# Kernel optimization log

Measured on AMD Instinct MI355X. Metric: run time of the kernel, lower is better.

The kernel has to match this reference:

```python
import jax, jax.numpy as jnp
import numpy as np
import math

B, T, C = 1, 4096, 2048
N_HEAD, N_KV = 16, 4
HD = C // N_HEAD            # 128
QPK = N_HEAD // N_KV        # 4
WINDOW = 1024
QKV_OUT = (N_HEAD + 2 * N_KV) * HD  # 3072


def setup_inputs() -> dict:
    key = jax.random.key(0)
    k1, k2, k3 = jax.random.split(key, 3)
    x = jax.random.normal(k1, (B, T, C), dtype=jnp.float32)
    W_attn = jax.random.normal(k2, (C, QKV_OUT), dtype=jnp.float32) * 0.02
    W_proj = jax.random.normal(k3, (C, C), dtype=jnp.float32) * 0.02
    # RoPE table: (T, HD//2, 2) = (cos, sin)
    inv_freq = 1.0 / (10000.0 ** (np.arange(0, HD, 2, dtype=np.float32) / HD))
    t = np.arange(T, dtype=np.float32)
    ang = np.outer(t, inv_freq)  # (T, HD//2)
    freqs_cis = jnp.asarray(np.stack([np.cos(ang), np.sin(ang)], axis=-1))
    return {"x": x, "freqs_cis": freqs_cis, "W_attn": W_attn, "W_proj": W_proj}


def apply_rope(xh, freqs_cis):
    # xh: (B, T, H, D); freqs_cis: (T, D//2, 2)
    b, t, h, d = xh.shape
    xs = xh.astype(jnp.float32).reshape(b, t, h, d // 2, 2)
    fc = freqs_cis.reshape(1, t, 1, d // 2, 2)
    re = xs[..., 0] * fc[..., 0] - xs[..., 1] * fc[..., 1]
    im = xs[..., 1] * fc[..., 0] + xs[..., 0] * fc[..., 1]
    return jnp.stack([re, im], axis=-1).reshape(b, t, h, d).astype(xh.dtype)


def reference(x, freqs_cis, W_attn, W_proj):
    qkv = x @ W_attn                                    # (B, T, 3072)
    tot = QPK + 2
    qkv = qkv.reshape(B, T, N_KV, tot, HD)
    qkv = jnp.transpose(qkv, (0, 2, 3, 1, 4))           # (B, n_kv, tot, T, hd)
    q = qkv[:, :, :QPK]                                 # (B, n_kv, qpk, T, hd)
    k = qkv[:, :, QPK:QPK + 1]
    v = qkv[:, :, QPK + 1:]
    # Faithful to torch: raw contiguous reshape (scrambles head/time layout)
    q = q.reshape(B, -1, N_HEAD, HD)                    # (B, T, n_head, hd)
    k = k.reshape(B, -1, N_KV, HD)
    v = v.reshape(B, -1, N_KV, HD)
    q = apply_rope(q, freqs_cis)
    k = apply_rope(k, freqs_cis)
    # GQA: physical repeat_interleave of K/V heads
    k = jnp.repeat(k, QPK, axis=2)                      # (B, T, n_head, hd)
    v = jnp.repeat(v, QPK, axis=2)
    q = jnp.transpose(q, (0, 2, 1, 3))                  # (B, n_head, T, hd)
    k = jnp.transpose(k, (0, 2, 1, 3))
    v = jnp.transpose(v, (0, 2, 1, 3))
    scores = jnp.einsum("bhqd,bhkd->bhqk", q, k) / math.sqrt(HD)
    # Symmetric band mask (triu(-w+1) * tril(w-1)): |i-j| <= w-1. NOT causal.
    i = jnp.arange(T)[:, None]
    j = jnp.arange(T)[None, :]
    band = jnp.abs(i - j) <= (WINDOW - 1)               # (T, T) bool
    scores = jnp.where(band[None, None], scores, -jnp.inf)
    probs = jax.nn.softmax(scores.astype(jnp.float32), axis=-1).astype(q.dtype)
    y = jnp.einsum("bhqk,bhkd->bhqd", probs, v)         # (B, n_head, T, hd)
    y = jnp.transpose(y, (0, 2, 1, 3)).reshape(B, T, C)
    return y @ W_proj
```

## Files before the change

kernel.cpp:

```cpp
#include <hip/hip_runtime.h>
#include <hip/hip_bf16.h>

typedef __attribute__((ext_vector_type(8))) short short8;
typedef __attribute__((ext_vector_type(4))) float f32x4;

static constexpr int Tt   = 4096;
static constexpr int Cc   = 2048;
static constexpr int NH   = 16;
static constexpr int HD   = 128;
static constexpr int QKVO = 3072;
static constexpr int W1   = 1023;

#define GLDS16(gp, lp)                                                        \
  __builtin_amdgcn_global_load_lds(                                           \
      (const __attribute__((address_space(1))) unsigned int*)(gp),            \
      (__attribute__((address_space(3))) unsigned int*)(lp), 16, 0, 0)

__global__ void cvt4(const float* __restrict__ in,
                     __hip_bfloat16* __restrict__ out, int n) {
  int i = (blockIdx.x * blockDim.x + threadIdx.x) * 4;
  if (i >= n) return;
  float4 v = *(const float4*)&in[i];
  union { ushort4 u; __hip_bfloat16 b[4]; } o;
  o.b[0] = __float2bfloat16(v.x);
  o.b[1] = __float2bfloat16(v.y);
  o.b[2] = __float2bfloat16(v.z);
  o.b[3] = __float2bfloat16(v.w);
  *(ushort4*)&out[i] = o.u;
}

__global__ void tconv(const float* __restrict__ W,
                      __hip_bfloat16* __restrict__ Wt, int K, int N) {
  __shared__ float tile[32][33];
  const int k0 = blockIdx.x * 32, n0 = blockIdx.y * 32;
  const int tx = threadIdx.x, ty = threadIdx.y;
#pragma unroll
  for (int r = 0; r < 4; ++r)
    tile[ty * 4 + r][tx] = W[(size_t)(k0 + ty * 4 + r) * N + n0 + tx];
  __syncthreads();
#pragma unroll
  for (int r = 0; r < 4; ++r)
    Wt[(size_t)(n0 + ty * 4 + r) * K + k0 + tx] =
        __float2bfloat16(tile[tx][ty * 4 + r]);
}

template <bool OUT_BF16>
__global__ __launch_bounds__(256) void gemm_bt(
    const __hip_bfloat16* __restrict__ A, const __hip_bfloat16* __restrict__ Bt,
    void* __restrict__ Cout, int M, int N, int K) {
  __shared__ __hip_bfloat16 As[128 * 32];
  __shared__ __hip_bfloat16 Bs[128 * 32];
  const int tid = threadIdx.x;
  const int lane = tid & 63, wid = tid >> 6;
  const int l15 = lane & 15, lhi = lane >> 4;
  const int m0 = blockIdx.y * 128, n0 = blockIdx.x * 128;
  const int wm = wid >> 1, wn = wid & 1;
  f32x4 acc[4][4] = {};
  for (int k0 = 0; k0 < K; k0 += 32) {
#pragma unroll
    for (int cc = 0; cc < 2; ++cc) {
      const int ebase = cc * 2048 + wid * 512;
      const int el = ebase + lane * 8;
      const int row = el >> 5, col = el & 31;
      GLDS16(A + (size_t)(m0 + row) * K + k0 + col, As + ebase);
      GLDS16(Bt + (size_t)(n0 + row) * K + k0 + col, Bs + ebase);
    }
    __syncthreads();
    short8 af[4], bfr[4];
#pragma unroll
    for (int i = 0; i < 4; ++i)
      af[i] = *(const short8*)&As[(wm * 64 + i * 16 + l15) * 32 + lhi * 8];
#pragma unroll
    for (int j = 0; j < 4; ++j)
      bfr[j] = *(const short8*)&Bs[(wn * 64 + j * 16 + l15) * 32 + lhi * 8];
#pragma unroll
    for (int i = 0; i < 4; ++i)
#pragma unroll
      for (int j = 0; j < 4; ++j)
        acc[i][j] = __builtin_amdgcn_mfma_f32_16x16x32_bf16(af[i], bfr[j],
                                                            acc[i][j], 0, 0, 0);
    __syncthreads();
  }
#pragma unroll
  for (int i = 0; i < 4; ++i)
#pragma unroll
    for (int r = 0; r < 4; ++r) {
      const int row = m0 + wm * 64 + i * 16 + lhi * 4 + r;
#pragma unroll
      for (int j = 0; j < 4; ++j) {
        const int col = n0 + wn * 64 + j * 16 + l15;
        if (OUT_BF16)
          ((__hip_bfloat16*)Cout)[(size_t)row * N + col] =
              __float2bfloat16(acc[i][j][r]);
        else
          ((float*)Cout)[(size_t)row * N + col] = acc[i][j][r];
      }
    }
}

__global__ void rope_scatter(const __hip_bfloat16* __restrict__ qkv,
                             const float* __restrict__ fc,
                             __hip_bfloat16* __restrict__ qb,
                             __hip_bfloat16* __restrict__ kb,
                             __hip_bfloat16* __restrict__ vb) {
  const int p = blockIdx.x * blockDim.x + threadIdx.x;
  const int t = blockIdx.y;
  const int c = p * 2;
  const int kv = c / 768;
  const int rem = c - kv * 768;
  const int slot = rem >> 7;
  const int d = rem & 127;
  const ushort2 xy = *(const ushort2*)&qkv[(size_t)t * QKVO + c];
  const float x0 = __bfloat162float(*(const __hip_bfloat16*)&xy.x);
  const float x1 = __bfloat162float(*(const __hip_bfloat16*)&xy.y);
  union { ushort2 uu; __hip_bfloat16 b[2]; } o;
  if (slot < 4) {
    const unsigned u = ((unsigned)kv << 14) | ((unsigned)slot << 12) | (unsigned)t;
    const int tp = u >> 4, h = u & 15;
    const float2 cs = *(const float2*)&fc[(size_t)tp * 128 + (d >> 1) * 2];
    o.b[0] = __float2bfloat16(x0 * cs.x - x1 * cs.y);
    o.b[1] = __float2bfloat16(x1 * cs.x + x0 * cs.y);
    *(ushort2*)&qb[(size_t)tp * Cc + h * HD + d] = o.uu;
  } else {
    const unsigned u2 = ((unsigned)kv << 12) | (unsigned)t;
    const int tp = u2 >> 2, hk = u2 & 3;
    if (slot == 4) {
      const float2 cs = *(const float2*)&fc[(size_t)tp * 128 + (d >> 1) * 2];
      o.b[0] = __float2bfloat16(x0 * cs.x - x1 * cs.y);
      o.b[1] = __float2bfloat16(x1 * cs.x + x0 * cs.y);
      *(ushort2*)&kb[(size_t)tp * 512 + hk * HD + d] = o.uu;
    } else {
      o.uu = xy;
      *(ushort2*)&vb[(size_t)tp * 512 + hk * HD + d] = o.uu;
    }
  }
}

__global__ __launch_bounds__(512) void attn_band(
    const __hip_bfloat16* __restrict__ qb, const __hip_bfloat16* __restrict__ kb,
    const __hip_bfloat16* __restrict__ vb, __hip_bfloat16* __restrict__ yb) {
  __shared__ __hip_bfloat16 kt[64 * 128];
  __shared__ __hip_bfloat16 vt[128 * 64];
  __shared__ __hip_bfloat16 pl[8][16 * 64];
  const int tid = threadIdx.x, lane = tid & 63, wid = tid >> 6;
  const int l15 = lane & 15, lhi = lane >> 4;
  const int q0 = blockIdx.x * 128, h = blockIdx.y;
  const int kvh = h >> 2;
  const int qrow = q0 + wid * 16 + l15;
  short8 aq[4];
#pragma unroll
  for (int kc = 0; kc < 4; ++kc)
    aq[kc] = *(const short8*)&qb[(size_t)qrow * Cc + h * HD + kc * 32 + lhi * 8];
  f32x4 o[8] = {};
  float mrow[4] = {-1e30f, -1e30f, -1e30f, -1e30f};
  float lrow[4] = {0.f, 0.f, 0.f, 0.f};
  const int js = (q0 - W1 > 0 ? q0 - W1 : 0) & ~63;
  const int jeu = q0 + 128 + W1;
  const int je = jeu < Tt ? jeu : Tt;
  const float scale = 0.08838834764831845f;
  char* ktc = (char*)kt;
  char* vtc = (char*)vt;
  char* plc = (char*)&pl[wid][0];
  for (int j0 = js; j0 < je; j0 += 64) {
    __syncthreads();
#pragma unroll
    for (int cc = 0; cc < 2; ++cc) {
      const int sb = (cc * 8 + wid) << 10;
      const int S = sb + lane * 16;
      const int row = S >> 8;
      const int colb = (S & 255) ^ ((row & 7) << 4);
      int jc = j0 + row;
      jc = jc < Tt - 1 ? jc : Tt - 1;
      GLDS16(kb + (size_t)jc * 512 + kvh * HD + (colb >> 1), ktc + sb);
    }
#pragma unroll
    for (int it = 0; it < 2; ++it) {
      const int d = tid & 127;
      const int jg = (tid >> 7) + it * 4;
      union { short8 v8; unsigned short u[8]; } pk;
#pragma unroll
      for (int q = 0; q < 8; ++q) {
        int jc = j0 + jg * 8 + q;
        jc = jc < Tt - 1 ? jc : Tt - 1;
        pk.u[q] = *(const unsigned short*)&vb[(size_t)jc * 512 + kvh * HD + d];
      }
      const int vbyt = (d * 128 + jg * 16) ^ ((d & 7) << 4);
      *(short8*)(vtc + vbyt) = pk.v8;
    }
    __syncthreads();
    f32x4 s[4] = {};
#pragma unroll
    for (int jt = 0; jt < 4; ++jt) {
      const int row = jt * 16 + l15;
      const int sw = (row & 7) << 4;
#pragma unroll
      for (int kc = 0; kc < 4; ++kc) {
        const short8 bk =
            *(const short8*)(ktc + row * 256 + ((kc * 64 + lhi * 16) ^ sw));
        s[jt] = __builtin_amdgcn_mfma_f32_16x16x32_bf16(aq[kc], bk, s[jt], 0, 0, 0);
      }
    }
    float val[4][4], pm[4];
#pragma unroll
    for (int jt = 0; jt < 4; ++jt)
#pragma unroll
      for (int r = 0; r < 4; ++r) {
        const int j = j0 + jt * 16 + l15;
        const int i = q0 + wid * 16 + lhi * 4 + r;
        const int diff = i > j ? i - j : j - i;
        const bool ok = (j < Tt) && (diff <= W1);
        val[jt][r] = ok ? s[jt][r] * scale : -1e30f;
      }
#pragma unroll
    for (int r = 0; r < 4; ++r) {
      float v = fmaxf(fmaxf(val[0][r], val[1][r]), fmaxf(val[2][r], val[3][r]));
      v = fmaxf(v, __shfl_xor(v, 1));
      v = fmaxf(v, __shfl_xor(v, 2));
      v = fmaxf(v, __shfl_xor(v, 4));
      v = fmaxf(v, __shfl_xor(v, 8));
      pm[r] = v;
    }
    float esc[4];
#pragma unroll
    for (int r = 0; r < 4; ++r) {
      const float mn = fmaxf(mrow[r], pm[r]);
      esc[r] = __expf(mrow[r] - mn);
      mrow[r] = mn;
    }
    float rs[4] = {0.f, 0.f, 0.f, 0.f};
#pragma unroll
    for (int jt = 0; jt < 4; ++jt)
#pragma unroll
      for (int r = 0; r < 4; ++r) {
        const float p = __expf(val[jt][r] - mrow[r]);
        rs[r] += p;
        const int row = lhi * 4 + r;
        const int b = row * 128 + (((jt * 16 + l15) * 2) ^ ((row & 7) << 4));
        *(__hip_bfloat16*)(plc + b) = __float2bfloat16(p);
      }
#pragma unroll
    for (int r = 0; r < 4; ++r) {
      float v = rs[r];
      v += __shfl_xor(v, 1);
      v += __shfl_xor(v, 2);
      v += __shfl_xor(v, 4);
      v += __shfl_xor(v, 8);
      lrow[r] = lrow[r] * esc[r] + v;
    }
#pragma unroll
    for (int dt = 0; dt < 8; ++dt)
#pragma unroll
      for (int r = 0; r < 4; ++r) o[dt][r] *= esc[r];
    const int psw = (l15 & 7) << 4;
    const short8 pa0 = *(const short8*)(plc + l15 * 128 + ((lhi * 16) ^ psw));
    const short8 pa1 = *(const short8*)(plc + l15 * 128 + ((64 + lhi * 16) ^ psw));
#pragma unroll
    for (int dt = 0; dt < 8; ++dt) {
      const int d = dt * 16 + l15;
      const int vsw = (d & 7) << 4;
      const short8 bv0 = *(const short8*)(vtc + d * 128 + ((lhi * 16) ^ vsw));
      const short8 bv1 = *(const short8*)(vtc + d * 128 + ((64 + lhi * 16) ^ vsw));
      o[dt] = __builtin_amdgcn_mfma_f32_16x16x32_bf16(pa0, bv0, o[dt], 0, 0, 0);
      o[dt] = __builtin_amdgcn_mfma_f32_16x16x32_bf16(pa1, bv1, o[dt], 0, 0, 0);
    }
  }
#pragma unroll
  for (int dt = 0; dt < 8; ++dt)
#pragma unroll
    for (int r = 0; r < 4; ++r) {
      const int i = q0 + wid * 16 + lhi * 4 + r;
      yb[(size_t)i * Cc + h * HD + dt * 16 + l15] =
          __float2bfloat16(o[dt][r] / lrow[r]);
    }
}

extern "C" void kernel_launch(void* const* d_in, const int* in_sizes, int n_in,
                              void* d_out, int out_size, void* d_ws,
                              size_t ws_size, hipStream_t stream) {
  const float* x = (const float*)d_in[0];
  const float* fc = (const float*)d_in[1];
  const float* Wa = (const float*)d_in[2];
  const float* Wp = (const float*)d_in[3];
  float* out = (float*)d_out;
  char* ws = (char*)d_ws;
  __hip_bfloat16* xb  = (__hip_bfloat16*)(ws);
  __hip_bfloat16* Wat = (__hip_bfloat16*)(ws + (16u << 20));
  __hip_bfloat16* Wpt = (__hip_bfloat16*)(ws + (28u << 20));
  __hip_bfloat16* qkv = (__hip_bfloat16*)(ws + (36u << 20));
  __hip_bfloat16* qb  = (__hip_bfloat16*)(ws);
  __hip_bfloat16* kb  = (__hip_bfloat16*)(ws + (16u << 20));
  __hip_bfloat16* vb  = (__hip_bfloat16*)(ws + (20u << 20));
  __hip_bfloat16* yb  = qkv;

  cvt4<<<dim3(Tt * Cc / 1024), 256, 0, stream>>>(x, xb, Tt * Cc);
  tconv<<<dim3(Cc / 32, QKVO / 32), dim3(32, 8), 0, stream>>>(Wa, Wat, Cc, QKVO);
  tconv<<<dim3(Cc / 32, Cc / 32), dim3(32, 8), 0, stream>>>(Wp, Wpt, Cc, Cc);
  gemm_bt<true><<<dim3(QKVO / 128, Tt / 128), 256, 0, stream>>>(
      xb, Wat, qkv, Tt, QKVO, Cc);
  rope_scatter<<<dim3(6, Tt), 256, 0, stream>>>(qkv, fc, qb, kb, vb);
  attn_band<<<dim3(Tt / 128, NH), 512, 0, stream>>>(qb, kb, vb, yb);
  gemm_bt<false><<<dim3(Cc / 128, Tt / 128), 256, 0, stream>>>(
      yb, Wpt, out, Tt, Cc, Cc);
}
```

Before: 463.3 us.

## Pre-transpose V, double-buffer K/V LDS tiles, and skip softmax rescale lazily

Adds a kernel that transposes V per KV head so attention can load V tiles with asynchronous global-to-LDS copies instead of scalar gathers. K and V tiles are double-buffered so the next tile's loads overlap the current tile's compute, with one barrier per iteration. The online softmax now rescales the accumulators only when the running max rises by more than a threshold, saving exp and multiply work. In exchange there is an extra transpose launch, more LDS use that may lower occupancy, and slightly looser numerical headroom from the lazy max.

```diff
diff --git a/kernel.cpp b/kernel.cpp
--- a/kernel.cpp
+++ b/kernel.cpp
@@ -42,6 +42,23 @@
   for (int r = 0; r < 4; ++r)
     Wt[(size_t)(n0 + ty * 4 + r) * K + k0 + tx] =
         __float2bfloat16(tile[tx][ty * 4 + r]);
+}
+
+__global__ void vtrans(const __hip_bfloat16* __restrict__ vb,
+                       __hip_bfloat16* __restrict__ vbt) {
+  __shared__ unsigned short tile[32][34];
+  const int t0 = blockIdx.x * 32, d0 = blockIdx.y * 32, kvh = blockIdx.z;
+  const int tx = threadIdx.x, ty = threadIdx.y;
+#pragma unroll
+  for (int r = 0; r < 4; ++r)
+    tile[ty * 4 + r][tx] =
+        *(const unsigned short*)&vb[(size_t)(t0 + ty * 4 + r) * 512 +
+                                    kvh * HD + d0 + tx];
+  __syncthreads();
+#pragma unroll
+  for (int r = 0; r < 4; ++r)
+    *(unsigned short*)&vbt[(size_t)kvh * 524288 + (size_t)(d0 + ty * 4 + r) * Tt +
+                           t0 + tx] = tile[tx][ty * 4 + r];
 }
 
 template <bool OUT_BF16>
@@ -138,9 +155,9 @@
 
 __global__ __launch_bounds__(512) void attn_band(
     const __hip_bfloat16* __restrict__ qb, const __hip_bfloat16* __restrict__ kb,
-    const __hip_bfloat16* __restrict__ vb, __hip_bfloat16* __restrict__ yb) {
-  __shared__ __hip_bfloat16 kt[64 * 128];
-  __shared__ __hip_bfloat16 vt[128 * 64];
+    const __hip_bfloat16* __restrict__ vbt, __hip_bfloat16* __restrict__ yb) {
+  __shared__ __hip_bfloat16 kt[2][64 * 128];
+  __shared__ __hip_bfloat16 vt[2][128 * 64];
   __shared__ __hip_bfloat16 pl[8][16 * 64];
   const int tid = threadIdx.x, lane = tid & 63, wid = tid >> 6;
   const int l15 = lane & 15, lhi = lane >> 4;
@@ -157,37 +174,44 @@
   const int js = (q0 - W1 > 0 ? q0 - W1 : 0) & ~63;
   const int jeu = q0 + 128 + W1;
   const int je = jeu < Tt ? jeu : Tt;
+  const int nt = (je - js + 63) >> 6;
   const float scale = 0.08838834764831845f;
-  char* ktc = (char*)kt;
-  char* vtc = (char*)vt;
+  char* ktb = (char*)kt;
+  char* vtb = (char*)vt;
   char* plc = (char*)&pl[wid][0];
-  for (int j0 = js; j0 < je; j0 += 64) {
-    __syncthreads();
+  const size_t vbase = (size_t)kvh * 524288;
+
+  auto stage = [&](int j0, int buf) {
+    char* kd = ktb + buf * 16384;
+    char* vd = vtb + buf * 16384;
 #pragma unroll
     for (int cc = 0; cc < 2; ++cc) {
       const int sb = (cc * 8 + wid) << 10;
-      const int S = sb + lane * 16;
-      const int row = S >> 8;
-      const int colb = (S & 255) ^ ((row & 7) << 4);
-      int jc = j0 + row;
-      jc = jc < Tt - 1 ? jc : Tt - 1;
-      GLDS16(kb + (size_t)jc * 512 + kvh * HD + (colb >> 1), ktc + sb);
-    }
-#pragma unroll
-    for (int it = 0; it < 2; ++it) {
-      const int d = tid & 127;
-      const int jg = (tid >> 7) + it * 4;
-      union { short8 v8; unsigned short u[8]; } pk;
-#pragma unroll
-      for (int q = 0; q < 8; ++q) {
-        int jc = j0 + jg * 8 + q;
+      {
+        const int S = sb + lane * 16;
+        const int row = S >> 8;
+        const int colb = (S & 255) ^ ((row & 7) << 4);
+        int jc = j0 + row;
         jc = jc < Tt - 1 ? jc : Tt - 1;
-        pk.u[q] = *(const unsigned short*)&vb[(size_t)jc * 512 + kvh * HD + d];
-      }
-      const int vbyt = (d * 128 + jg * 16) ^ ((d & 7) << 4);
-      *(short8*)(vtc + vbyt) = pk.v8;
-    }
+        GLDS16(kb + (size_t)jc * 512 + kvh * HD + (colb >> 1), kd + sb);
+      }
+      {
+        const int S = sb + lane * 16;
+        const int row = S >> 7;
+        const int colb = (S & 127) ^ ((row & 7) << 4);
+        GLDS16(vbt + vbase + (size_t)row * Tt + j0 + (colb >> 1), vd + sb);
+      }
+    }
+  };
+
+  stage(js, 0);
+  int cur = 0;
+  for (int t = 0; t < nt; ++t) {
+    const int j0 = js + t * 64;
     __syncthreads();
+    if (t + 1 < nt) stage(j0 + 64, cur ^ 1);
+    char* ktc = ktb + cur * 16384;
+    char* vtc = vtb + cur * 16384;
     f32x4 s[4] = {};
 #pragma unroll
     for (int jt = 0; jt < 4; ++jt) {
@@ -220,12 +244,19 @@
       v = fmaxf(v, __shfl_xor(v, 8));
       pm[r] = v;
     }
-    float esc[4];
-#pragma unroll
-    for (int r = 0; r < 4; ++r) {
-      const float mn = fmaxf(mrow[r], pm[r]);
-      esc[r] = __expf(mrow[r] - mn);
-      mrow[r] = mn;
+    float need = 0.f;
+#pragma unroll
+    for (int r = 0; r < 4; ++r) need = fmaxf(need, pm[r] - mrow[r]);
+    if (!__all(need <= 8.0f)) {
+#pragma unroll
+      for (int r = 0; r < 4; ++r) {
+        const float mn = fmaxf(mrow[r], pm[r]);
+        const float esc = __expf(mrow[r] - mn);
+        mrow[r] = mn;
+        lrow[r] *= esc;
+#pragma unroll
+        for (int dt = 0; dt < 8; ++dt) o[dt][r] *= esc;
+      }
     }
     float rs[4] = {0.f, 0.f, 0.f, 0.f};
 #pragma unroll
@@ -245,12 +276,8 @@
       v += __shfl_xor(v, 2);
       v += __shfl_xor(v, 4);
       v += __shfl_xor(v, 8);
-      lrow[r] = lrow[r] * esc[r] + v;
-    }
-#pragma unroll
-    for (int dt = 0; dt < 8; ++dt)
-#pragma unroll
-      for (int r = 0; r < 4; ++r) o[dt][r] *= esc[r];
+      lrow[r] += v;
+    }
     const int psw = (l15 & 7) << 4;
     const short8 pa0 = *(const short8*)(plc + l15 * 128 + ((lhi * 16) ^ psw));
     const short8 pa1 = *(const short8*)(plc + l15 * 128 + ((64 + lhi * 16) ^ psw));
@@ -263,6 +290,7 @@
       o[dt] = __builtin_amdgcn_mfma_f32_16x16x32_bf16(pa0, bv0, o[dt], 0, 0, 0);
       o[dt] = __builtin_amdgcn_mfma_f32_16x16x32_bf16(pa1, bv1, o[dt], 0, 0, 0);
     }
+    cur ^= 1;
   }
 #pragma unroll
   for (int dt = 0; dt < 8; ++dt)
@@ -290,6 +318,7 @@
   __hip_bfloat16* qb  = (__hip_bfloat16*)(ws);
   __hip_bfloat16* kb  = (__hip_bfloat16*)(ws + (16u << 20));
   __hip_bfloat16* vb  = (__hip_bfloat16*)(ws + (20u << 20));
+  __hip_bfloat16* vbt = (__hip_bfloat16*)(ws + (24u << 20));
   __hip_bfloat16* yb  = qkv;
 
   cvt4<<<dim3(Tt * Cc / 1024), 256, 0, stream>>>(x, xb, Tt * Cc);
@@ -298,7 +327,8 @@
   gemm_bt<true><<<dim3(QKVO / 128, Tt / 128), 256, 0, stream>>>(
       xb, Wat, qkv, Tt, QKVO, Cc);
   rope_scatter<<<dim3(6, Tt), 256, 0, stream>>>(qkv, fc, qb, kb, vb);
-  attn_band<<<dim3(Tt / 128, NH), 512, 0, stream>>>(qb, kb, vb, yb);
+  vtrans<<<dim3(Tt / 32, HD / 32, 4), dim3(32, 8), 0, stream>>>(vb, vbt);
+  attn_band<<<dim3(Tt / 128, NH), 512, 0, stream>>>(qb, kb, vbt, yb);
   gemm_bt<false><<<dim3(Cc / 128, Tt / 128), 256, 0, stream>>>(
       yb, Wpt, out, Tt, Cc, Cc);
 }
```

New measurement: 460.0 us. About the same (-0.7%).
